# Performance work log

Measured on AMD Instinct MI355X. Metric: run time of the kernel, lower is better.

## Reference

```python
import jax, jax.numpy as jnp
import numpy as np

B, C, H, W = 8, 256, 64, 64
NH, FF, L, K = 8, 1024, 3, 64
THR = 0.5
DH = C // NH
SCALE = 1.0 / float(np.sqrt(DH))
N = H * W


def setup_inputs() -> dict:
    key = jax.random.key(0)
    ks = jax.random.split(key, 16)
    s = 0.02
    rn = lambda k, shape: (jax.random.normal(k, shape, jnp.float32) * s)
    return {
        "x": jax.random.normal(ks[0], (B, C, H, W), jnp.float32),
        "y": jax.random.normal(ks[1], (B, C, H, W), jnp.float32),
        "proj_w": rn(ks[2], (C, 2 * C)), "proj_b": rn(ks[3], (C,)),
        "sal_w": rn(ks[4], (1, C)), "sal_b": rn(ks[5], (1,)),
        "soft_w": rn(ks[6], (2, K, C)), "soft_b": rn(ks[7], (2, K)),
        "attn_in_w": rn(ks[8], (2, L, 3 * C, C)), "attn_in_b": rn(ks[9], (2, L, 3 * C)),
        "attn_out_w": rn(ks[10], (2, L, C, C)), "attn_out_b": rn(ks[11], (2, L, C)),
        "n1_g": jnp.ones((2, L, C), jnp.float32), "n1_b": jnp.zeros((2, L, C), jnp.float32),
        "ffn_w1": rn(ks[12], (2, L, FF, C)), "ffn_b1": rn(ks[13], (2, L, FF)),
        "ffn_w2": rn(ks[14], (2, L, C, FF)), "ffn_b2": rn(ks[15], (2, L, C)),
        "n2_g": jnp.ones((2, L, C), jnp.float32), "n2_b": jnp.zeros((2, L, C), jnp.float32),
    }


def _ln(t, g, b, eps=1e-5):
    m = t.mean(-1, keepdims=True)
    v = ((t - m) ** 2).mean(-1, keepdims=True)
    return (t - m) / jnp.sqrt(v + eps) * g + b


def _layers(q, kv, p, side):
    # q: [B,N,C] pixel queries, kv: [B,K,C] soft-pooled tokens
    for l in range(L):
        iw, ib = p["attn_in_w"][side, l], p["attn_in_b"][side, l]
        qq = (q @ iw[:C].T + ib[:C]).reshape(B, -1, NH, DH)
        kk = (kv @ iw[C:2 * C].T + ib[C:2 * C]).reshape(B, K, NH, DH)
        vv = (kv @ iw[2 * C:].T + ib[2 * C:]).reshape(B, K, NH, DH)
        att = jax.nn.softmax(jnp.einsum('bnhd,bkhd->bhnk', qq, kk) * SCALE, axis=-1)
        o = jnp.einsum('bhnk,bkhd->bnhd', att, vv).reshape(B, -1, C)
        o = o @ p["attn_out_w"][side, l].T + p["attn_out_b"][side, l]
        q = _ln(q + o, p["n1_g"][side, l], p["n1_b"][side, l])
        h = jax.nn.relu(q @ p["ffn_w1"][side, l].T + p["ffn_b1"][side, l])
        h = h @ p["ffn_w2"][side, l].T + p["ffn_b2"][side, l]
        q = _ln(q + h, p["n2_g"][side, l], p["n2_b"][side, l])
    return q


def _forward(x, y, proj_w, proj_b, sal_w, sal_b, soft_w, soft_b,
             attn_in_w, attn_in_b, attn_out_w, attn_out_b, n1_g, n1_b,
             ffn_w1, ffn_b1, ffn_w2, ffn_b2, n2_g, n2_b):
    p = dict(attn_in_w=attn_in_w, attn_in_b=attn_in_b, attn_out_w=attn_out_w,
             attn_out_b=attn_out_b, n1_g=n1_g, n1_b=n1_b, ffn_w1=ffn_w1,
             ffn_b1=ffn_b1, ffn_w2=ffn_w2, ffn_b2=ffn_b2, n2_g=n2_g, n2_b=n2_b)
    xc = jnp.concatenate([x, y], axis=1)                                  # [B,2C,H,W]
    feat = jnp.einsum('oc,bchw->bohw', proj_w, xc) + proj_b[None, :, None, None]
    sal = jnp.einsum('oc,bchw->bohw', sal_w, feat) + sal_b[None, :, None, None]  # [B,1,H,W]
    heat = jax.nn.sigmoid(sal)
    fg_mask = (heat >= THR).reshape(B, 1, N)
    bg_mask = (heat < 1.0 - THR).reshape(B, 1, N)
    fmap = feat.reshape(B, C, N)
    q0 = fmap.transpose(0, 2, 1)                                          # [B,N,C]
    out = fmap
    for side, hm in ((0, heat), (1, 1.0 - heat)):
        wf = feat * hm                                                    # [B,C,H,W]
        sw = (jnp.einsum('kc,bchw->bkhw', soft_w[side], wf)
              + soft_b[side][None, :, None, None]).reshape(B, K, N)       # [B,K,N]
        pool = jnp.einsum('bkn,bcn->bkc', sw, wf.reshape(B, C, N))        # [B,K,C]
        qs = _layers(q0, pool, p, side)                                   # [B,N,C]
        mask = fg_mask if side == 0 else bg_mask
        out = jnp.where(mask, qs.transpose(0, 2, 1), out)
    # per-image skip: if no fg or no bg pixels, keep original feature
    valid = fg_mask.any(axis=(1, 2)) & bg_mask.any(axis=(1, 2))           # [B]
    out = jnp.where(valid[:, None, None], out, fmap)
    return out.reshape(B, C, H, W)


def reference(x, y, proj_w, proj_b, sal_w, sal_b, soft_w, soft_b,
              attn_in_w, attn_in_b, attn_out_w, attn_out_b, n1_g, n1_b,
              ffn_w1, ffn_b1, ffn_w2, ffn_b2, n2_g, n2_b):
    return _forward(x, y, proj_w, proj_b, sal_w, sal_b, soft_w, soft_b,
                    attn_in_w, attn_in_b, attn_out_w, attn_out_b, n1_g, n1_b,
                    ffn_w1, ffn_b1, ffn_w2, ffn_b2, n2_g, n2_b)
```

## Files before the change

### kernel.cpp

```cpp
#include <hip/hip_runtime.h>
#include <stdint.h>

#define B_ 8
#define C_ 256
#define N_ 4096
#define K_ 64
#define NH_ 8
#define FF_ 1024
#define L_ 3
#define M_ (B_*N_)
#define SCALE_ 0.17677669529663687f

typedef float f32x4 __attribute__((ext_vector_type(4)));
typedef __bf16 v8bf __attribute__((ext_vector_type(8)));

__device__ __forceinline__ float b2f(unsigned short h){
  union { uint32_t u; float f; } v; v.u = ((uint32_t)h) << 16; return v.f;
}
__device__ __forceinline__ unsigned short f2b(float f){
  union { float f; uint32_t u; } v; v.f = f;
  uint32_t r = v.u + 0x7fffu + ((v.u >> 16) & 1u);
  return (unsigned short)(r >> 16);
}
__device__ __forceinline__ void gload_lds16(const void* g, void* l){
  __builtin_amdgcn_global_load_lds(
      (const __attribute__((address_space(1))) unsigned int*)g,
      (__attribute__((address_space(3))) unsigned int*)l, 16, 0, 0);
}
__device__ __forceinline__ void unpack8(uint4 v, float* o){
  o[0]=b2f((unsigned short)(v.x & 0xffff)); o[1]=b2f((unsigned short)(v.x >> 16));
  o[2]=b2f((unsigned short)(v.y & 0xffff)); o[3]=b2f((unsigned short)(v.y >> 16));
  o[4]=b2f((unsigned short)(v.z & 0xffff)); o[5]=b2f((unsigned short)(v.z >> 16));
  o[6]=b2f((unsigned short)(v.w & 0xffff)); o[7]=b2f((unsigned short)(v.w >> 16));
}

__global__ __launch_bounds__(256) void k_f32_to_bf16(const float* __restrict__ src,
                                                     unsigned short* __restrict__ dst, int n){
  int i4 = (blockIdx.x*256 + threadIdx.x)*4;
  if (i4 >= n) return;
  float4 v = *(const float4*)(src + i4);
  uint32_t p0 = (uint32_t)f2b(v.x) | ((uint32_t)f2b(v.y) << 16);
  uint32_t p1 = (uint32_t)f2b(v.z) | ((uint32_t)f2b(v.w) << 16);
  *(uint2*)(dst + i4) = make_uint2(p0, p1);
}

__global__ __launch_bounds__(256) void k_build_xcT(const float* __restrict__ x,
                                                   const float* __restrict__ y,
                                                   unsigned short* __restrict__ xcT){
  __shared__ float t[32][33];
  int b = blockIdx.z;
  int n0 = blockIdx.x*32, c0 = blockIdx.y*32;
  int tx = threadIdx.x, ty = threadIdx.y;
  const float* src = (c0 < 256) ? (x + ((size_t)b*256 + c0)*N_)
                                : (y + ((size_t)b*256 + (c0-256))*N_);
  #pragma unroll
  for (int i = 0; i < 4; i++){
    int cl = ty*4 + i;
    t[cl][tx] = src[(size_t)cl*N_ + n0 + tx];
  }
  __syncthreads();
  #pragma unroll
  for (int i = 0; i < 4; i++){
    int nl = ty*4 + i;
    xcT[((size_t)b*N_ + n0 + nl)*512 + c0 + tx] = f2b(t[tx][nl]);
  }
}

__global__ __launch_bounds__(256) void k_featmir(const float* __restrict__ featT,
                                                 unsigned short* __restrict__ featbf,
                                                 unsigned short* __restrict__ featC){
  __shared__ float t[32][33];
  int b = blockIdx.z;
  int n0 = blockIdx.x*32, c0 = blockIdx.y*32;
  int tx = threadIdx.x, ty = threadIdx.y;
  #pragma unroll
  for (int i = 0; i < 4; i++){
    int nl = ty*4 + i;
    size_t m = (size_t)b*N_ + n0 + nl;
    float v = featT[m*256 + c0 + tx];
    t[nl][tx] = v;
    featbf[m*256 + c0 + tx] = f2b(v);
  }
  __syncthreads();
  #pragma unroll
  for (int i = 0; i < 4; i++){
    int cl = ty*4 + i;
    featC[((size_t)b*256 + c0 + cl)*(size_t)N_ + n0 + tx] = f2b(t[tx][cl]);
  }
}

__global__ __launch_bounds__(512) void k_compute_u(const float* __restrict__ sal_w,
                                                   const float* __restrict__ proj_w,
                                                   const float* __restrict__ proj_b,
                                                   const float* __restrict__ sal_b,
                                                   double* __restrict__ u){
  int c2 = threadIdx.x;
  double acc = 0.0;
  for (int c = 0; c < 256; ++c)
    acc += (double)sal_w[c] * (double)proj_w[(size_t)c*512 + c2];
  u[c2] = acc;
  if (c2 == 0){
    double s0 = (double)sal_b[0];
    for (int c = 0; c < 256; ++c) s0 += (double)sal_w[c] * (double)proj_b[c];
    u[512] = s0;
  }
}

__global__ __launch_bounds__(256) void k_sal_part(const float* __restrict__ x,
                                                  const float* __restrict__ y,
                                                  const double* __restrict__ u,
                                                  double* __restrict__ part){
  int pix = blockIdx.x*256 + threadIdx.x;
  int cc = blockIdx.y;
  int b = pix >> 12, n = pix & 4095;
  int c0 = cc*32;
  const float* src = (c0 < 256) ? (x + ((size_t)b*256 + c0)*N_ + n)
                                : (y + ((size_t)b*256 + (c0-256))*N_ + n);
  const double* uu = u + c0;
  double acc = 0.0;
  #pragma unroll 8
  for (int c = 0; c < 32; ++c) acc += uu[c] * (double)src[(size_t)c*N_];
  part[(size_t)cc*32768 + pix] = acc;
}

__global__ __launch_bounds__(256) void k_sal_red(const double* __restrict__ part,
                                                 const double* __restrict__ u,
                                                 float* __restrict__ heat,
                                                 int* __restrict__ counts){
  int pix = blockIdx.x*256 + threadIdx.x;
  int b = pix >> 12;
  double acc = u[512];
  #pragma unroll
  for (int cc = 0; cc < 16; cc++) acc += part[(size_t)cc*32768 + pix];
  float hf = (float)(1.0 / (1.0 + exp(-acc)));
  heat[pix] = hf;
  unsigned long long mfg = __ballot(hf >= 0.5f);
  unsigned long long mbg = __ballot(hf < 0.5f);
  if ((threadIdx.x & 63) == 0){
    atomicAdd(&counts[b*2+0], (int)__popcll(mfg));
    atomicAdd(&counts[b*2+1], (int)__popcll(mbg));
  }
}

template<int EPI>
__global__ __launch_bounds__(256) void k_gemm_bt(
    const unsigned short* __restrict__ A, const unsigned short* __restrict__ W,
    const float* __restrict__ bias, void* __restrict__ out,
    int M, int N, int K){
  __shared__ unsigned short smem[2][2][128*64];
  int tid = threadIdx.x;
  int w = tid >> 6, l = tid & 63;
  int m0 = blockIdx.x * 128, n0 = blockIdx.y * 128;
  int wr = w >> 1, wc = w & 1;
  int lr = l & 15, lk = l >> 4;
  f32x4 acc[4][4] = {};
  int nt = K >> 6;
  #pragma unroll
  for (int i = 0; i < 4; i++){
    int idx = i*256 + tid;
    int row = idx >> 3, su = ((idx & 7) ^ (row & 7))*8;
    gload_lds16(A + (size_t)(m0+row)*K + su, &smem[0][0][idx*8]);
    gload_lds16(W + (size_t)(n0+row)*K + su, &smem[0][1][idx*8]);
  }
  __syncthreads();
  for (int t = 0; t < nt; ++t){
    int cur = t & 1;
    if (t + 1 < nt){
      int k0 = (t + 1) << 6;
      #pragma unroll
      for (int i = 0; i < 4; i++){
        int idx = i*256 + tid;
        int row = idx >> 3, su = ((idx & 7) ^ (row & 7))*8;
        gload_lds16(A + (size_t)(m0+row)*K + k0 + su, &smem[cur^1][0][idx*8]);
        gload_lds16(W + (size_t)(n0+row)*K + k0 + su, &smem[cur^1][1][idx*8]);
      }
    }
    const unsigned short* ldsA = smem[cur][0];
    const unsigned short* ldsB = smem[cur][1];
    #pragma unroll
    for (int kk = 0; kk < 2; kk++){
      v8bf af[4], bfr[4];
      #pragma unroll
      for (int f = 0; f < 4; f++){
        int ra = wr*64 + f*16 + lr;
        int rb2 = wc*64 + f*16 + lr;
        int u = kk*4 + lk;
        af[f]  = *(const v8bf*)(&ldsA[ra*64 + ((u ^ (ra&7))<<3)]);
        bfr[f] = *(const v8bf*)(&ldsB[rb2*64 + ((u ^ (rb2&7))<<3)]);
      }
      #pragma unroll
      for (int fi = 0; fi < 4; fi++)
        #pragma unroll
        for (int fj = 0; fj < 4; fj++)
          acc[fi][fj] = __builtin_amdgcn_mfma_f32_16x16x32_bf16(af[fi], bfr[fj], acc[fi][fj], 0, 0, 0);
    }
    __syncthreads();
  }
  if (EPI == 1 || EPI == 2){
    unsigned short* st = &smem[0][0][0];
    #pragma unroll
    for (int fj = 0; fj < 4; fj++){
      int col = wc*64 + fj*16 + lr;
      float bv = bias[n0 + col];
      #pragma unroll
      for (int fi = 0; fi < 4; fi++){
        int rl = wr*64 + fi*16 + lk*4;
        #pragma unroll
        for (int r = 0; r < 4; r++){
          float v = acc[fi][fj][r] + bv;
          if (EPI == 1) v = fmaxf(v, 0.f);
          st[(rl + r)*136 + col] = f2b(v);
        }
      }
    }
    __syncthreads();
    #pragma unroll
    for (int it = 0; it < 8; it++){
      int idx = it*256 + tid;
      int row = idx >> 4, c8 = (idx & 15)*8;
      *(uint4*)((unsigned short*)out + (size_t)(m0+row)*N + n0 + c8)
          = *(const uint4*)&st[row*136 + c8];
    }
  } else {
    #pragma unroll
    for (int fj = 0; fj < 4; fj++){
      int col = n0 + wc*64 + fj*16 + lr;
      float bv = bias[col];
      #pragma unroll
      for (int fi = 0; fi < 4; fi++){
        int rb = m0 + wr*64 + fi*16 + lk*4;
        #pragma unroll
        for (int r = 0; r < 4; r++){
          float v = acc[fi][fj][r] + bv;
          if (EPI == 3){
            int row = rb + r;
            ((unsigned short*)out)[((size_t)(row>>6)*256 + col)*64 + (row&63)] = f2b(v);
          } else {
            ((float*)out)[(size_t)(rb + r)*N + col] = v;
          }
        }
      }
    }
  }
}

__global__ __launch_bounds__(256) void k_kv(
    const unsigned short* __restrict__ pool, const unsigned short* __restrict__ iw,
    const float* __restrict__ ib, unsigned short* __restrict__ kk_bf,
    unsigned short* __restrict__ vvT_bf){
  __shared__ unsigned short smem[2][2][128*64];
  int tid = threadIdx.x;
  int w = tid >> 6, l = tid & 63;
  int m0 = blockIdx.x * 128, n0 = blockIdx.y * 128;
  int isv = blockIdx.z;
  const unsigned short* W = iw + (size_t)(isv ? 512 : 256)*256;
  const float* bias = ib + (isv ? 512 : 256);
  int wr = w >> 1, wc = w & 1;
  int lr = l & 15, lk = l >> 4;
  f32x4 acc[4][4] = {};
  #pragma unroll
  for (int i = 0; i < 4; i++){
    int idx = i*256 + tid;
    int row = idx >> 3, su = ((idx & 7) ^ (row & 7))*8;
    gload_lds16(pool + (size_t)(m0+row)*256 + su, &smem[0][0][idx*8]);
    gload_lds16(W + (size_t)(n0+row)*256 + su, &smem[0][1][idx*8]);
  }
  __syncthreads();
  for (int t = 0; t < 4; ++t){
    int cur = t & 1;
    if (t + 1 < 4){
      int k0 = (t + 1) << 6;
      #pragma unroll
      for (int i = 0; i < 4; i++){
        int idx = i*256 + tid;
        int row = idx >> 3, su = ((idx & 7) ^ (row & 7))*8;
        gload_lds16(pool + (size_t)(m0+row)*256 + k0 + su, &smem[cur^1][0][idx*8]);
        gload_lds16(W + (size_t)(n0+row)*256 + k0 + su, &smem[cur^1][1][idx*8]);
      }
    }
    const unsigned short* ldsA = smem[cur][0];
    const unsigned short* ldsB = smem[cur][1];
    #pragma unroll
    for (int kk = 0; kk < 2; kk++){
      v8bf af[4], bfr[4];
      #pragma unroll
      for (int f = 0; f < 4; f++){
        int ra = wr*64 + f*16 + lr;
        int rb2 = wc*64 + f*16 + lr;
        int u = kk*4 + lk;
        af[f]  = *(const v8bf*)(&ldsA[ra*64 + ((u ^ (ra&7))<<3)]);
        bfr[f] = *(const v8bf*)(&ldsB[rb2*64 + ((u ^ (rb2&7))<<3)]);
      }
      #pragma unroll
      for (int fi = 0; fi < 4; fi++)
        #pragma unroll
        for (int fj = 0; fj < 4; fj++)
          acc[fi][fj] = __builtin_amdgcn_mfma_f32_16x16x32_bf16(af[fi], bfr[fj], acc[fi][fj], 0, 0, 0);
    }
    __syncthreads();
  }
  #pragma unroll
  for (int fj = 0; fj < 4; fj++){
    int col = n0 + wc*64 + fj*16 + lr;
    float bv = bias[col];
    #pragma unroll
    for (int fi = 0; fi < 4; fi++){
      int rb = m0 + wr*64 + fi*16 + lk*4;
      #pragma unroll
      for (int r = 0; r < 4; r++){
        float v = acc[fi][fj][r] + bv;
        int row = rb + r;
        if (isv)
          vvT_bf[((size_t)(row>>6)*256 + col)*64 + (row&63)] = f2b(v);
        else
          kk_bf[(size_t)row*256 + col] = f2b(v);
      }
    }
  }
}

template<int RF32>
__global__ __launch_bounds__(512) void k_gemm_ln(
    const unsigned short* __restrict__ A, const unsigned short* __restrict__ W,
    const float* __restrict__ bias, const void* __restrict__ resid,
    const float* __restrict__ g, const float* __restrict__ bta,
    unsigned short* __restrict__ qout){
  __shared__ unsigned short smem[49152];
  int tid = threadIdx.x;
  int w = tid >> 6, l = tid & 63;
  int m0 = blockIdx.x * 128;
  int wm = w >> 2, wf = w & 3;
  int lr = l & 15, lk = l >> 4;
  f32x4 acc[4][4] = {};
  #pragma unroll
  for (int i = 0; i < 2; i++){
    int idx = i*512 + tid;
    int row = idx >> 3, su = ((idx & 7) ^ (row & 7))*8;
    gload_lds16(A + (size_t)(m0+row)*256 + su, &smem[idx*8]);
  }
  #pragma unroll
  for (int i = 0; i < 4; i++){
    int idx = i*512 + tid;
    int row = idx >> 3, su = ((idx & 7) ^ (row & 7))*8;
    gload_lds16(W + (size_t)row*256 + su, &smem[8192 + idx*8]);
  }
  __syncthreads();
  for (int t = 0; t < 4; ++t){
    int cur = t & 1;
    if (t + 1 < 4){
      int k0 = (t + 1) << 6;
      unsigned short* bA = smem + (cur^1)*24576;
      unsigned short* bB = bA + 8192;
      #pragma unroll
      for (int i = 0; i < 2; i++){
        int idx = i*512 + tid;
        int row = idx >> 3, su = ((idx & 7) ^ (row & 7))*8;
        gload_lds16(A + (size_t)(m0+row)*256 + k0 + su, &bA[idx*8]);
      }
      #pragma unroll
      for (int i = 0; i < 4; i++){
        int idx = i*512 + tid;
        int row = idx >> 3, su = ((idx & 7) ^ (row & 7))*8;
        gload_lds16(W + (size_t)row*256 + k0 + su, &bB[idx*8]);
      }
    }
    const unsigned short* bA = smem + cur*24576;
    const unsigned short* bB = bA + 8192;
    #pragma unroll
    for (int kk = 0; kk < 2; kk++){
      v8bf af[4], wb[4];
      int u = kk*4 + lk;
      #pragma unroll
      for (int f = 0; f < 4; f++){
        int ra = wm*64 + f*16 + lr;
        af[f] = *(const v8bf*)&bA[ra*64 + ((u ^ (ra&7))<<3)];
      }
      #pragma unroll
      for (int f = 0; f < 4; f++){
        int rc = wf*64 + f*16 + lr;
        wb[f] = *(const v8bf*)&bB[rc*64 + ((u ^ (rc&7))<<3)];
      }
      #pragma unroll
      for (int fi = 0; fi < 4; fi++)
        #pragma unroll
        for (int fc = 0; fc < 4; fc++)
          acc[fi][fc] = __builtin_amdgcn_mfma_f32_16x16x32_bf16(af[fi], wb[fc], acc[fi][fc], 0, 0, 0);
    }
    __syncthreads();
  }
  unsigned short* st = smem;
  #pragma unroll
  for (int fc = 0; fc < 4; fc++){
    int col = wf*64 + fc*16 + lr;
    float bv = bias[col];
    #pragma unroll
    for (int fi = 0; fi < 4; fi++){
      int rl = wm*64 + fi*16 + lk*4;
      #pragma unroll
      for (int r = 0; r < 4; r++)
        st[(rl + r)*264 + col] = f2b(acc[fi][fc][r] + bv);
    }
  }
  __syncthreads();
  int row = tid >> 2, seg = tid & 3;
  float xv[64];
  #pragma unroll
  for (int j = 0; j < 8; j++){
    int cu = seg*8 + j;
    uint4 dv = *(const uint4*)&st[row*264 + cu*8];
    float dd[8];
    unpack8(dv, dd);
    if (RF32){
      const float* rp = (const float*)resid + (size_t)(m0+row)*256 + cu*8;
      float4 r0 = *(const float4*)rp, r1 = *(const float4*)(rp + 4);
      xv[j*8+0] = r0.x + dd[0]; xv[j*8+1] = r0.y + dd[1];
      xv[j*8+2] = r0.z + dd[2]; xv[j*8+3] = r0.w + dd[3];
      xv[j*8+4] = r1.x + dd[4]; xv[j*8+5] = r1.y + dd[5];
      xv[j*8+6] = r1.z + dd[6]; xv[j*8+7] = r1.w + dd[7];
    } else {
      uint4 rv = *(const uint4*)((const unsigned short*)resid + (size_t)(m0+row)*256 + cu*8);
      float rr[8];
      unpack8(rv, rr);
      #pragma unroll
      for (int e = 0; e < 8; e++) xv[j*8+e] = rr[e] + dd[e];
    }
  }
  float s = 0.f, q = 0.f;
  #pragma unroll
  for (int i2 = 0; i2 < 64; i2++){ s += xv[i2]; q += xv[i2]*xv[i2]; }
  s += __shfl_xor(s, 1); s += __shfl_xor(s, 2);
  q += __shfl_xor(q, 1); q += __shfl_xor(q, 2);
  float mean = s * (1.0f/256.0f);
  float rstd = 1.0f / sqrtf(q*(1.0f/256.0f) - mean*mean + 1e-5f);
  #pragma unroll
  for (int j = 0; j < 8; j++){
    int c0 = seg*64 + j*8;
    float4 g0 = *(const float4*)(g + c0), g1 = *(const float4*)(g + c0 + 4);
    float4 b0 = *(const float4*)(bta + c0), b1 = *(const float4*)(bta + c0 + 4);
    float y0 = (xv[j*8+0]-mean)*rstd*g0.x + b0.x;
    float y1 = (xv[j*8+1]-mean)*rstd*g0.y + b0.y;
    float y2 = (xv[j*8+2]-mean)*rstd*g0.z + b0.z;
    float y3 = (xv[j*8+3]-mean)*rstd*g0.w + b0.w;
    float y4 = (xv[j*8+4]-mean)*rstd*g1.x + b1.x;
    float y5 = (xv[j*8+5]-mean)*rstd*g1.y + b1.y;
    float y6 = (xv[j*8+6]-mean)*rstd*g1.z + b1.z;
    float y7 = (xv[j*8+7]-mean)*rstd*g1.w + b1.w;
    uint4 ov;
    ov.x = (uint32_t)f2b(y0) | ((uint32_t)f2b(y1)<<16);
    ov.y = (uint32_t)f2b(y2) | ((uint32_t)f2b(y3)<<16);
    ov.z = (uint32_t)f2b(y4) | ((uint32_t)f2b(y5)<<16);
    ov.w = (uint32_t)f2b(y6) | ((uint32_t)f2b(y7)<<16);
    *(uint4*)(qout + (size_t)(m0+row)*256 + c0) = ov;
  }
}

__global__ __launch_bounds__(512) void k_ffn(
    const unsigned short* __restrict__ qb, const unsigned short* __restrict__ W1g,
    const float* __restrict__ b1g, const unsigned short* __restrict__ W2g,
    const float* __restrict__ b2g, const float* __restrict__ n2g,
    const float* __restrict__ n2b, unsigned short* __restrict__ qout){
  __shared__ unsigned short smem[73728];
  unsigned short* sA  = smem;
  unsigned short* sW1 = smem + 32768;
  unsigned short* sW2 = smem + 49152;
  unsigned short* sH  = smem + 65536;
  int tid = threadIdx.x;
  int w = tid >> 6, l = tid & 63;
  int m0 = blockIdx.x * 128;
  int wm = w >> 2, wf = w & 3;
  int lr = l & 15, lk = l >> 4;

  #pragma unroll
  for (int i = 0; i < 8; i++){
    int idx = i*512 + tid;
    int row = idx >> 5, gu = idx & 31;
    int su = (gu & 24) | ((gu & 7) ^ (row & 7));
    gload_lds16(qb + (size_t)(m0+row)*256 + su*8, &sA[idx*8]);
  }
  #pragma unroll
  for (int i = 0; i < 4; i++){
    int idx = i*512 + tid;
    int row = idx >> 5, gu = idx & 31;
    int su = (gu & 24) | ((gu & 7) ^ (row & 7));
    gload_lds16(W1g + (size_t)row*256 + su*8, &sW1[idx*8]);
  }
  #pragma unroll
  for (int i = 0; i < 4; i++){
    int idx = i*512 + tid;
    int row = idx >> 3, gu = idx & 7;
    int su = gu ^ (row & 7);
    gload_lds16(W2g + (size_t)row*1024 + su*8, &sW2[idx*8]);
  }
  __syncthreads();

  f32x4 acc[4][4] = {};
  for (int cc = 0; cc < 16; ++cc){
    f32x4 hacc[4] = {};
    #pragma unroll
    for (int ks = 0; ks < 8; ks++){
      int gu = ks*4 + lk;
      int rf = wf*16 + lr;
      v8bf bf1 = *(const v8bf*)&sW1[rf*256 + (((gu & 24) | ((gu & 7) ^ (rf & 7)))<<3)];
      #pragma unroll
      for (int f = 0; f < 4; f++){
        int ra = wm*64 + f*16 + lr;
        v8bf af = *(const v8bf*)&sA[ra*256 + (((gu & 24) | ((gu & 7) ^ (ra & 7)))<<3)];
        hacc[f] = __builtin_amdgcn_mfma_f32_16x16x32_bf16(af, bf1, hacc[f], 0, 0, 0);
      }
    }
    {
      int fc = wf*16 + lr;
      float b1v = b1g[cc*64 + fc];
      #pragma unroll
      for (int fi = 0; fi < 4; fi++){
        int mr0 = wm*64 + fi*16 + lk*4;
        #pragma unroll
        for (int r = 0; r < 4; r++){
          float v = fmaxf(hacc[fi][r] + b1v, 0.f);
          int mr = mr0 + r;
          int key = (mr ^ (mr >> 3)) & 7;
          sH[mr*64 + (((fc >> 3) ^ key)<<3) + (fc & 7)] = f2b(v);
        }
      }
    }
    __syncthreads();
    if (cc + 1 < 16){
      int f0n = (cc+1)*64;
      #pragma unroll
      for (int i = 0; i < 4; i++){
        int idx = i*512 + tid;
        int row = idx >> 5, gu = idx & 31;
        int su = (gu & 24) | ((gu & 7) ^ (row & 7));
        gload_lds16(W1g + (size_t)(f0n+row)*256 + su*8, &sW1[idx*8]);
      }
    }
    #pragma unroll
    for (int ks2 = 0; ks2 < 2; ks2++){
      int gu = ks2*4 + lk;
      v8bf ha[4], wb[4];
      #pragma unroll
      for (int f = 0; f < 4; f++){
        int rh = wm*64 + f*16 + lr;
        int key = (rh ^ (rh >> 3)) & 7;
        ha[f] = *(const v8bf*)&sH[rh*64 + ((gu ^ key)<<3)];
      }
      #pragma unroll
      for (int f = 0; f < 4; f++){
        int rc = wf*64 + f*16 + lr;
        wb[f] = *(const v8bf*)&sW2[rc*64 + ((gu ^ (rc & 7))<<3)];
      }
      #pragma unroll
      for (int fi = 0; fi < 4; fi++)
        #pragma unroll
        for (int fc = 0; fc < 4; fc++)
          acc[fi][fc] = __builtin_amdgcn_mfma_f32_16x16x32_bf16(ha[fi], wb[fc], acc[fi][fc], 0, 0, 0);
    }
    __syncthreads();
    if (cc + 1 < 16){
      int f0n = (cc+1)*64;
      #pragma unroll
      for (int i = 0; i < 4; i++){
        int idx = i*512 + tid;
        int row = idx >> 3, gu = idx & 7;
        int su = gu ^ (row & 7);
        gload_lds16(W2g + (size_t)row*1024 + f0n + su*8, &sW2[idx*8]);
      }
    }
  }

  unsigned short* st = smem + 32768;
  #pragma unroll
  for (int fc = 0; fc < 4; fc++){
    int col = wf*64 + fc*16 + lr;
    float bv = b2g[col];
    #pragma unroll
    for (int fi = 0; fi < 4; fi++){
      int rl = wm*64 + fi*16 + lk*4;
      #pragma unroll
      for (int r = 0; r < 4; r++)
        st[(rl + r)*264 + col] = f2b(acc[fi][fc][r] + bv);
    }
  }
  __syncthreads();
  int row = tid >> 2, seg = tid & 3;
  float xv[64];
  #pragma unroll
  for (int j = 0; j < 8; j++){
    int cu = seg*8 + j;
    int su = (cu & 24) | ((cu & 7) ^ (row & 7));
    uint4 rv = *(const uint4*)&sA[row*256 + su*8];
    uint4 dv = *(const uint4*)&st[row*264 + cu*8];
    float rr[8], dd[8];
    unpack8(rv, rr); unpack8(dv, dd);
    #pragma unroll
    for (int e = 0; e < 8; e++) xv[j*8+e] = rr[e] + dd[e];
  }
  float s = 0.f, q = 0.f;
  #pragma unroll
  for (int i2 = 0; i2 < 64; i2++){ s += xv[i2]; q += xv[i2]*xv[i2]; }
  s += __shfl_xor(s, 1); s += __shfl_xor(s, 2);
  q += __shfl_xor(q, 1); q += __shfl_xor(q, 2);
  float mean = s * (1.0f/256.0f);
  float rstd = 1.0f / sqrtf(q*(1.0f/256.0f) - mean*mean + 1e-5f);
  #pragma unroll
  for (int j = 0; j < 8; j++){
    int c0 = seg*64 + j*8;
    float4 g0 = *(const float4*)(n2g + c0), g1 = *(const float4*)(n2g + c0 + 4);
    float4 b0 = *(const float4*)(n2b + c0), b1 = *(const float4*)(n2b + c0 + 4);
    float y0 = (xv[j*8+0]-mean)*rstd*g0.x + b0.x;
    float y1 = (xv[j*8+1]-mean)*rstd*g0.y + b0.y;
    float y2 = (xv[j*8+2]-mean)*rstd*g0.z + b0.z;
    float y3 = (xv[j*8+3]-mean)*rstd*g0.w + b0.w;
    float y4 = (xv[j*8+4]-mean)*rstd*g1.x + b1.x;
    float y5 = (xv[j*8+5]-mean)*rstd*g1.y + b1.y;
    float y6 = (xv[j*8+6]-mean)*rstd*g1.z + b1.z;
    float y7 = (xv[j*8+7]-mean)*rstd*g1.w + b1.w;
    uint4 ov;
    ov.x = (uint32_t)f2b(y0) | ((uint32_t)f2b(y1)<<16);
    ov.y = (uint32_t)f2b(y2) | ((uint32_t)f2b(y3)<<16);
    ov.z = (uint32_t)f2b(y4) | ((uint32_t)f2b(y5)<<16);
    ov.w = (uint32_t)f2b(y6) | ((uint32_t)f2b(y7)<<16);
    *(uint4*)(qout + (size_t)(m0+row)*256 + c0) = ov;
  }
}

__global__ __launch_bounds__(256) void k_swh(const float* __restrict__ g_all,
                                             const float* __restrict__ heat,
                                             const float* __restrict__ soft_b,
                                             unsigned short* __restrict__ swh){
  __shared__ float gl[64*129];
  __shared__ float hml[64];
  int tid = threadIdx.x;
  int blk = blockIdx.x;
  size_t m0 = (size_t)blk*64;
  int b = (int)(m0 >> 12), n0 = (int)(m0 & 4095);
  #pragma unroll
  for (int i = 0; i < 32; i++){
    int idx = i*256 + tid;
    int row = idx >> 7, col = idx & 127;
    gl[row*129 + col] = g_all[(m0 + row)*128 + col];
  }
  if (tid < 64) hml[tid] = heat[(size_t)b*4096 + n0 + tid];
  __syncthreads();
  int k = tid >> 2, j0 = (tid & 3)*16;
  #pragma unroll
  for (int s = 0; s < 2; s++){
    float sb = soft_b[s*64 + k];
    unsigned short vals[16];
    #pragma unroll
    for (int j = 0; j < 16; j++){
      int n = j0 + j;
      float h = hml[n];
      float hm = s ? (1.0f - h) : h;
      vals[j] = f2b((gl[n*129 + s*64 + k]*hm + sb)*hm);
    }
    unsigned short* dst = swh + (((size_t)b*2 + s)*64 + k)*4096 + n0 + j0;
    uint4 o0, o1;
    o0.x = vals[0] | ((uint32_t)vals[1]<<16);  o0.y = vals[2] | ((uint32_t)vals[3]<<16);
    o0.z = vals[4] | ((uint32_t)vals[5]<<16);  o0.w = vals[6] | ((uint32_t)vals[7]<<16);
    o1.x = vals[8] | ((uint32_t)vals[9]<<16);  o1.y = vals[10]| ((uint32_t)vals[11]<<16);
    o1.z = vals[12]| ((uint32_t)vals[13]<<16); o1.w = vals[14]| ((uint32_t)vals[15]<<16);
    *(uint4*)dst = o0;
    *(uint4*)(dst + 8) = o1;
  }
}

__global__ __launch_bounds__(256) void k_poolgemm(
    const unsigned short* __restrict__ swh, const unsigned short* __restrict__ featC,
    float* __restrict__ pp){
  __shared__ unsigned short ldsA[128*64];
  __shared__ unsigned short ldsB[128*64];
  int tid = threadIdx.x;
  int w = tid >> 6, l = tid & 63;
  int kc = blockIdx.x, nt = blockIdx.y, b = blockIdx.z;
  int wr = w >> 1, wc = w & 1;
  int lr = l & 15, lk = l >> 4;
  const unsigned short* A = swh  + (size_t)b*128*4096 + kc*512;
  const unsigned short* W = featC + ((size_t)b*256 + nt*128)*4096 + kc*512;
  f32x4 acc[4][4] = {};
  for (int k0 = 0; k0 < 512; k0 += 64){
    #pragma unroll
    for (int i = 0; i < 4; i++){
      int idx = i*256 + tid;
      int row = idx >> 3, su = (idx & 7) ^ (row & 7);
      gload_lds16(A + (size_t)row*4096 + k0 + su*8, &ldsA[idx*8]);
    }
    #pragma unroll
    for (int i = 0; i < 4; i++){
      int idx = i*256 + tid;
      int row = idx >> 3, su = (idx & 7) ^ (row & 7);
      gload_lds16(W + (size_t)row*4096 + k0 + su*8, &ldsB[idx*8]);
    }
    __syncthreads();
    #pragma unroll
    for (int kk = 0; kk < 2; kk++){
      v8bf af[4], bfr[4];
      #pragma unroll
      for (int f = 0; f < 4; f++){
        int ra = wr*64 + f*16 + lr;
        int rb2 = wc*64 + f*16 + lr;
        int u = kk*4 + lk;
        af[f]  = *(const v8bf*)(&ldsA[ra*64 + ((u ^ (ra&7))<<3)]);
        bfr[f] = *(const v8bf*)(&ldsB[rb2*64 + ((u ^ (rb2&7))<<3)]);
      }
      #pragma unroll
      for (int fi = 0; fi < 4; fi++)
        #pragma unroll
        for (int fj = 0; fj < 4; fj++)
          acc[fi][fj] = __builtin_amdgcn_mfma_f32_16x16x32_bf16(af[fi], bfr[fj], acc[fi][fj], 0, 0, 0);
    }
    __syncthreads();
  }
  float* dst = pp + ((size_t)kc*8 + b)*128*256;
  #pragma unroll
  for (int fj = 0; fj < 4; fj++){
    int col = nt*128 + wc*64 + fj*16 + lr;
    #pragma unroll
    for (int fi = 0; fi < 4; fi++){
      int rb = wr*64 + fi*16 + lk*4;
      #pragma unroll
      for (int r = 0; r < 4; r++)
        dst[(size_t)(rb + r)*256 + col] = acc[fi][fj][r];
    }
  }
}

__global__ __launch_bounds__(256) void k_pool2b(const float* __restrict__ pp,
                                                unsigned short* __restrict__ pool_bf_s){
  int bk = blockIdx.x, side = blockIdx.y, c = threadIdx.x;
  int b = bk >> 6, k = bk & 63;
  float s = 0.f;
  #pragma unroll
  for (int kc = 0; kc < 8; kc++)
    s += pp[(((size_t)kc*8 + b)*128 + side*64 + k)*256 + c];
  pool_bf_s[((size_t)side*512 + bk)*256 + c] = f2b(s);
}

__global__ __launch_bounds__(256) void k_attn2(
    const unsigned short* __restrict__ qq, const unsigned short* __restrict__ kk,
    const unsigned short* __restrict__ vvT, unsigned short* __restrict__ obf){
  __shared__ unsigned short sk[64*256];
  __shared__ unsigned short svT[256*64];
  __shared__ unsigned short sp[4][16*64];
  __shared__ unsigned short sow[4][16*32];
  int tid = threadIdx.x, w = tid >> 6, l = tid & 63;
  int blk = blockIdx.x, b = blk >> 6;
  int l15 = l & 15, lg = l >> 4;
  const uint4* ksrc = (const uint4*)(kk + (size_t)b*64*256);
  #pragma unroll
  for (int i = 0; i < 8; i++){
    int u = i*256 + tid;
    int row = u >> 5, j = u & 31;
    *(uint4*)&sk[row*256 + ((j ^ (row&7))<<3)] = ksrc[u];
  }
  const uint4* vsrc = (const uint4*)(vvT + (size_t)b*256*64);
  #pragma unroll
  for (int i = 0; i < 8; i++){
    int u = i*256 + tid;
    int row = u >> 3, j = u & 7;
    *(uint4*)&svT[row*64 + ((j ^ (row&7))<<3)] = vsrc[u];
  }
  __syncthreads();
  size_t qrow = (size_t)blk*64 + w*16 + l15;
  for (int h = 0; h < 8; h++){
    v8bf aq = *(const v8bf*)(qq + qrow*256 + h*32 + lg*8);
    f32x4 s[4];
    #pragma unroll
    for (int kt = 0; kt < 4; kt++){
      int row = kt*16 + l15;
      v8bf bk = *(const v8bf*)&sk[row*256 + (((h*4 + lg) ^ (row&7))<<3)];
      f32x4 z = {};
      s[kt] = __builtin_amdgcn_mfma_f32_16x16x32_bf16(aq, bk, z, 0, 0, 0);
    }
    #pragma unroll
    for (int r = 0; r < 4; r++){
      float v0 = s[0][r]*SCALE_, v1 = s[1][r]*SCALE_;
      float v2 = s[2][r]*SCALE_, v3 = s[3][r]*SCALE_;
      float mx = fmaxf(fmaxf(v0, v1), fmaxf(v2, v3));
      mx = fmaxf(mx, __shfl_xor(mx, 1));
      mx = fmaxf(mx, __shfl_xor(mx, 2));
      mx = fmaxf(mx, __shfl_xor(mx, 4));
      mx = fmaxf(mx, __shfl_xor(mx, 8));
      float e0 = __expf(v0-mx), e1 = __expf(v1-mx);
      float e2 = __expf(v2-mx), e3 = __expf(v3-mx);
      float sum = e0+e1+e2+e3;
      sum += __shfl_xor(sum, 1); sum += __shfl_xor(sum, 2);
      sum += __shfl_xor(sum, 4); sum += __shfl_xor(sum, 8);
      float inv = 1.0f/sum;
      s[0][r] = e0*inv; s[1][r] = e1*inv; s[2][r] = e2*inv; s[3][r] = e3*inv;
    }
    #pragma unroll
    for (int kt = 0; kt < 4; kt++){
      int colu = kt*2 + (l15>>3);
      #pragma unroll
      for (int r = 0; r < 4; r++){
        int row = lg*4 + r;
        sp[w][row*64 + ((colu ^ (row&7))<<3) + (l&7)] = f2b(s[kt][r]);
      }
    }
    f32x4 o[2] = {};
    #pragma unroll
    for (int k2 = 0; k2 < 2; k2++){
      v8bf pa = *(const v8bf*)&sp[w][l15*64 + (((k2*4 + lg) ^ (l15&7))<<3)];
      #pragma unroll
      for (int dt = 0; dt < 2; dt++){
        int vrow = h*32 + dt*16 + l15;
        v8bf bv = *(const v8bf*)&svT[vrow*64 + (((k2*4 + lg) ^ (vrow&7))<<3)];
        o[dt] = __builtin_amdgcn_mfma_f32_16x16x32_bf16(pa, bv, o[dt], 0, 0, 0);
      }
    }
    #pragma unroll
    for (int dt = 0; dt < 2; dt++)
      #pragma unroll
      for (int r = 0; r < 4; r++)
        sow[w][(lg*4 + r)*32 + dt*16 + l15] = f2b(o[dt][r]);
    uint4 ov = *(const uint4*)&sow[w][l15*32 + lg*8];
    *(uint4*)(obf + qrow*256 + h*32 + lg*8) = ov;
  }
}

__global__ __launch_bounds__(256) void k_select(
    const unsigned short* __restrict__ qA, const unsigned short* __restrict__ qB,
    const float* __restrict__ featT, const float* __restrict__ heat,
    const int* __restrict__ counts, float* __restrict__ out){
  __shared__ float t[32][33];
  int b = blockIdx.z;
  int n0 = blockIdx.x*32, c0 = blockIdx.y*32;
  int tx = threadIdx.x, ty = threadIdx.y;
  bool valid = (counts[b*2] > 0) && (counts[b*2+1] > 0);
  #pragma unroll
  for (int i = 0; i < 4; i++){
    int nl = ty*4+i;
    size_t m = (size_t)b*4096 + n0 + nl;
    float v;
    if (!valid) v = featT[m*256 + c0 + tx];
    else {
      bool fg = heat[(size_t)b*4096 + n0 + nl] >= 0.5f;
      v = fg ? b2f(qA[m*256 + c0 + tx]) : b2f(qB[m*256 + c0 + tx]);
    }
    t[nl][tx] = v;
  }
  __syncthreads();
  #pragma unroll
  for (int i = 0; i < 4; i++){
    int cl = ty*4+i;
    out[((size_t)b*256 + c0 + cl)*4096 + n0 + tx] = t[tx][cl];
  }
}

extern "C" void kernel_launch(void* const* d_in, const int* in_sizes, int n_in,
                              void* d_out, int out_size, void* d_ws, size_t ws_size,
                              hipStream_t stream){
  const float* x         = (const float*)d_in[0];
  const float* y         = (const float*)d_in[1];
  const float* proj_w    = (const float*)d_in[2];
  const float* proj_b    = (const float*)d_in[3];
  const float* sal_w     = (const float*)d_in[4];
  const float* sal_b     = (const float*)d_in[5];
  const float* soft_w    = (const float*)d_in[6];
  const float* soft_b    = (const float*)d_in[7];
  const float* attn_in_w = (const float*)d_in[8];
  const float* attn_in_b = (const float*)d_in[9];
  const float* attn_out_w= (const float*)d_in[10];
  const float* attn_out_b= (const float*)d_in[11];
  const float* n1_g      = (const float*)d_in[12];
  const float* n1_b      = (const float*)d_in[13];
  const float* ffn_w1    = (const float*)d_in[14];
  const float* ffn_b1    = (const float*)d_in[15];
  const float* ffn_w2    = (const float*)d_in[16];
  const float* ffn_b2    = (const float*)d_in[17];
  const float* n2_g      = (const float*)d_in[18];
  const float* n2_b      = (const float*)d_in[19];
  float* out = (float*)d_out;

  char* p = (char*)d_ws;
  auto alloc = [&](size_t bytes){ char* r = p; p += (bytes + 255) & ~(size_t)255; return r; };
  unsigned short* hbf   = (unsigned short*)alloc((size_t)M_*FF_*2);
  unsigned short* xcT   = hbf;
  unsigned short* qq_bf = hbf;
  float* featT = (float*)alloc((size_t)M_*C_*4);
  unsigned short* qAb = (unsigned short*)alloc((size_t)M_*C_*2);
  unsigned short* swh = qAb;
  unsigned short* qBb = (unsigned short*)alloc((size_t)M_*C_*2);
  unsigned short* obf = (unsigned short*)alloc((size_t)M_*C_*2);
  unsigned short* featC = obf;
  unsigned short* featbf = (unsigned short*)alloc((size_t)M_*C_*2);
  unsigned short* tmpb = (unsigned short*)alloc((size_t)M_*C_*2);
  float* g_all = (float*)tmpb;
  float* pp    = (float*)alloc((size_t)8*8*128*256*4);
  double* salp = (double*)pp;
  unsigned short* pool_bf_s = (unsigned short*)alloc((size_t)2*512*256*2);
  unsigned short* kk_bf = (unsigned short*)alloc((size_t)B_*K_*C_*2);
  unsigned short* vvT_bf= (unsigned short*)alloc((size_t)B_*C_*K_*2);
  float* heat = (float*)alloc((size_t)B_*N_*4);
  double* u   = (double*)alloc(513*8);
  int* counts = (int*)alloc(64);
  float* zbias = (float*)alloc(512);
  unsigned short* projw_bf = (unsigned short*)alloc((size_t)C_*512*2);
  unsigned short* aiw_bf = (unsigned short*)alloc((size_t)2*L_*768*C_*2);
  unsigned short* aow_bf = (unsigned short*)alloc((size_t)2*L_*C_*C_*2);
  unsigned short* f1w_bf = (unsigned short*)alloc((size_t)2*L_*FF_*C_*2);
  unsigned short* f2w_bf = (unsigned short*)alloc((size_t)2*L_*C_*FF_*2);
  unsigned short* sw2_bf = (unsigned short*)alloc((size_t)2*K_*C_*2);

  hipMemsetAsync(counts, 0, 64, stream);
  hipMemsetAsync(zbias, 0, 512, stream);
  k_compute_u<<<1, 512, 0, stream>>>(sal_w, proj_w, proj_b, sal_b, u);
  k_sal_part<<<dim3(128, 16), 256, 0, stream>>>(x, y, u, salp);
  k_sal_red<<<128, 256, 0, stream>>>(salp, u, heat, counts);

  auto conv = [&](const float* s, unsigned short* d, size_t n){
    k_f32_to_bf16<<<(unsigned)((n/4 + 255)/256), 256, 0, stream>>>(s, d, (int)n);
  };
  conv(proj_w,     projw_bf, (size_t)C_*512);
  conv(attn_in_w,  aiw_bf,   (size_t)2*L_*768*C_);
  conv(attn_out_w, aow_bf,   (size_t)2*L_*C_*C_);
  conv(ffn_w1,     f1w_bf,   (size_t)2*L_*FF_*C_);
  conv(ffn_w2,     f2w_bf,   (size_t)2*L_*C_*FF_);
  conv(soft_w,     sw2_bf,   (size_t)2*K_*C_);

  k_build_xcT<<<dim3(N_/32, 512/32, B_), dim3(32,8), 0, stream>>>(x, y, xcT);
  k_gemm_bt<0><<<dim3(M_/128, C_/128), 256, 0, stream>>>(xcT, projw_bf, proj_b, featT, M_, C_, 512);
  k_featmir<<<dim3(N_/32, C_/32, B_), dim3(32,8), 0, stream>>>(featT, featbf, featC);

  k_gemm_bt<0><<<dim3(M_/128, 1), 256, 0, stream>>>(featbf, sw2_bf, zbias, g_all, M_, 128, C_);
  k_swh<<<M_/64, 256, 0, stream>>>(g_all, heat, soft_b, swh);
  k_poolgemm<<<dim3(8, 2, B_), 256, 0, stream>>>(swh, featC, pp);
  k_pool2b<<<dim3(512, 2), 256, 0, stream>>>(pp, pool_bf_s);

  for (int side = 0; side < 2; ++side){
    unsigned short* qb = side ? qBb : qAb;
    const unsigned short* poolS = pool_bf_s + (size_t)side*512*256;
    for (int lyr = 0; lyr < L_; ++lyr){
      int sl = side*L_ + lyr;
      const unsigned short* iw = aiw_bf + (size_t)sl*768*C_;
      const float* ib = attn_in_b + (size_t)sl*768;
      const unsigned short* qin = (lyr == 0) ? featbf : qb;
      k_gemm_bt<2><<<dim3(M_/128, C_/128), 256, 0, stream>>>(qin, iw, ib, qq_bf, M_, C_, C_);
      k_kv<<<dim3(4, 2, 2), 256, 0, stream>>>(poolS, iw, ib, kk_bf, vvT_bf);
      k_attn2<<<M_/64, 256, 0, stream>>>(qq_bf, kk_bf, vvT_bf, obf);
      if (lyr == 0)
        k_gemm_ln<1><<<M_/128, 512, 0, stream>>>(obf, aow_bf + (size_t)sl*C_*C_,
            attn_out_b + (size_t)sl*C_, featT, n1_g + (size_t)sl*C_, n1_b + (size_t)sl*C_, qb);
      else
        k_gemm_ln<0><<<M_/128, 512, 0, stream>>>(obf, aow_bf + (size_t)sl*C_*C_,
            attn_out_b + (size_t)sl*C_, qb, n1_g + (size_t)sl*C_, n1_b + (size_t)sl*C_, qb);
      k_ffn<<<M_/128, 512, 0, stream>>>(qb, f1w_bf + (size_t)sl*FF_*C_, ffn_b1 + (size_t)sl*FF_,
                                        f2w_bf + (size_t)sl*C_*FF_, ffn_b2 + (size_t)sl*C_,
                                        n2_g + (size_t)sl*C_, n2_b + (size_t)sl*C_, qb);
    }
  }
  k_select<<<dim3(N_/32, C_/32, B_), dim3(32,8), 0, stream>>>(qAb, qBb, featT, heat, counts, out);
}
```

Measured before the change: 917.9 us.

## Split FFN residual+LayerNorm into separate kernel and stage outputs through LDS

Removes the fused residual-add and LayerNorm epilogue from the FFN kernel. The FFN kernel now writes its bias-added output to a temporary buffer, and a new per-row wave kernel (k_ln2) does the residual add and LayerNorm. The gemm_ln epilogue and the FFN store now stage results in LDS and write them out as coalesced rows, and the sH swizzle key is simplified. The goal is lower register pressure and better stores in the FFN kernel. The cost is an extra launch plus a full round trip of the activation tensor through global memory for each layer.

```diff
diff --git a/kernel.cpp b/kernel.cpp
--- a/kernel.cpp
+++ b/kernel.cpp
@@ -437,28 +437,30 @@
     int c0 = seg*64 + j*8;
     float4 g0 = *(const float4*)(g + c0), g1 = *(const float4*)(g + c0 + 4);
     float4 b0 = *(const float4*)(bta + c0), b1 = *(const float4*)(bta + c0 + 4);
-    float y0 = (xv[j*8+0]-mean)*rstd*g0.x + b0.x;
-    float y1 = (xv[j*8+1]-mean)*rstd*g0.y + b0.y;
-    float y2 = (xv[j*8+2]-mean)*rstd*g0.z + b0.z;
-    float y3 = (xv[j*8+3]-mean)*rstd*g0.w + b0.w;
-    float y4 = (xv[j*8+4]-mean)*rstd*g1.x + b1.x;
-    float y5 = (xv[j*8+5]-mean)*rstd*g1.y + b1.y;
-    float y6 = (xv[j*8+6]-mean)*rstd*g1.z + b1.z;
-    float y7 = (xv[j*8+7]-mean)*rstd*g1.w + b1.w;
     uint4 ov;
-    ov.x = (uint32_t)f2b(y0) | ((uint32_t)f2b(y1)<<16);
-    ov.y = (uint32_t)f2b(y2) | ((uint32_t)f2b(y3)<<16);
-    ov.z = (uint32_t)f2b(y4) | ((uint32_t)f2b(y5)<<16);
-    ov.w = (uint32_t)f2b(y6) | ((uint32_t)f2b(y7)<<16);
-    *(uint4*)(qout + (size_t)(m0+row)*256 + c0) = ov;
+    ov.x = (uint32_t)f2b((xv[j*8+0]-mean)*rstd*g0.x + b0.x)
+         | ((uint32_t)f2b((xv[j*8+1]-mean)*rstd*g0.y + b0.y) << 16);
+    ov.y = (uint32_t)f2b((xv[j*8+2]-mean)*rstd*g0.z + b0.z)
+         | ((uint32_t)f2b((xv[j*8+3]-mean)*rstd*g0.w + b0.w) << 16);
+    ov.z = (uint32_t)f2b((xv[j*8+4]-mean)*rstd*g1.x + b1.x)
+         | ((uint32_t)f2b((xv[j*8+5]-mean)*rstd*g1.y + b1.y) << 16);
+    ov.w = (uint32_t)f2b((xv[j*8+6]-mean)*rstd*g1.z + b1.z)
+         | ((uint32_t)f2b((xv[j*8+7]-mean)*rstd*g1.w + b1.w) << 16);
+    *(uint4*)&st[row*264 + c0] = ov;
+  }
+  __syncthreads();
+  #pragma unroll
+  for (int it = 0; it < 8; it++){
+    int idx = it*512 + tid;
+    int rw = idx >> 5, c8 = (idx & 31)*8;
+    *(uint4*)(qout + (size_t)(m0+rw)*256 + c8) = *(const uint4*)&st[rw*264 + c8];
   }
 }
 
 __global__ __launch_bounds__(512) void k_ffn(
     const unsigned short* __restrict__ qb, const unsigned short* __restrict__ W1g,
     const float* __restrict__ b1g, const unsigned short* __restrict__ W2g,
-    const float* __restrict__ b2g, const float* __restrict__ n2g,
-    const float* __restrict__ n2b, unsigned short* __restrict__ qout){
+    const float* __restrict__ b2g, unsigned short* __restrict__ outb){
   __shared__ unsigned short smem[73728];
   unsigned short* sA  = smem;
   unsigned short* sW1 = smem + 32768;
@@ -467,28 +469,29 @@
   int tid = threadIdx.x;
   int w = tid >> 6, l = tid & 63;
   int m0 = blockIdx.x * 128;
-  int wm = w >> 2, wf = w & 3;
+  int wm = w >> 2;
+  int wf = w & 3;
   int lr = l & 15, lk = l >> 4;
 
   #pragma unroll
   for (int i = 0; i < 8; i++){
     int idx = i*512 + tid;
-    int row = idx >> 5, gu = idx & 31;
-    int su = (gu & 24) | ((gu & 7) ^ (row & 7));
+    int row = idx >> 5, g = idx & 31;
+    int su = (g & 24) | ((g & 7) ^ (row & 7));
     gload_lds16(qb + (size_t)(m0+row)*256 + su*8, &sA[idx*8]);
   }
   #pragma unroll
   for (int i = 0; i < 4; i++){
     int idx = i*512 + tid;
-    int row = idx >> 5, gu = idx & 31;
-    int su = (gu & 24) | ((gu & 7) ^ (row & 7));
+    int row = idx >> 5, g = idx & 31;
+    int su = (g & 24) | ((g & 7) ^ (row & 7));
     gload_lds16(W1g + (size_t)row*256 + su*8, &sW1[idx*8]);
   }
   #pragma unroll
   for (int i = 0; i < 4; i++){
     int idx = i*512 + tid;
-    int row = idx >> 3, gu = idx & 7;
-    int su = gu ^ (row & 7);
+    int row = idx >> 3, g = idx & 7;
+    int su = g ^ (row & 7);
     gload_lds16(W2g + (size_t)row*1024 + su*8, &sW2[idx*8]);
   }
   __syncthreads();
@@ -498,13 +501,13 @@
     f32x4 hacc[4] = {};
     #pragma unroll
     for (int ks = 0; ks < 8; ks++){
-      int gu = ks*4 + lk;
+      int g = ks*4 + lk;
       int rf = wf*16 + lr;
-      v8bf bf1 = *(const v8bf*)&sW1[rf*256 + (((gu & 24) | ((gu & 7) ^ (rf & 7)))<<3)];
+      v8bf bf1 = *(const v8bf*)&sW1[rf*256 + (((g & 24) | ((g & 7) ^ (rf & 7)))<<3)];
       #pragma unroll
       for (int f = 0; f < 4; f++){
         int ra = wm*64 + f*16 + lr;
-        v8bf af = *(const v8bf*)&sA[ra*256 + (((gu & 24) | ((gu & 7) ^ (ra & 7)))<<3)];
+        v8bf af = *(const v8bf*)&sA[ra*256 + (((g & 24) | ((g & 7) ^ (ra & 7)))<<3)];
         hacc[f] = __builtin_amdgcn_mfma_f32_16x16x32_bf16(af, bf1, hacc[f], 0, 0, 0);
       }
     }
@@ -518,8 +521,7 @@
         for (int r = 0; r < 4; r++){
           float v = fmaxf(hacc[fi][r] + b1v, 0.f);
           int mr = mr0 + r;
-          int key = (mr ^ (mr >> 3)) & 7;
-          sH[mr*64 + (((fc >> 3) ^ key)<<3) + (fc & 7)] = f2b(v);
+          sH[mr*64 + (((fc >> 3) ^ (mr & 7))<<3) + (fc & 7)] = f2b(v);
         }
       }
     }
@@ -529,25 +531,24 @@
       #pragma unroll
       for (int i = 0; i < 4; i++){
         int idx = i*512 + tid;
-        int row = idx >> 5, gu = idx & 31;
-        int su = (gu & 24) | ((gu & 7) ^ (row & 7));
+        int row = idx >> 5, g = idx & 31;
+        int su = (g & 24) | ((g & 7) ^ (row & 7));
         gload_lds16(W1g + (size_t)(f0n+row)*256 + su*8, &sW1[idx*8]);
       }
     }
     #pragma unroll
     for (int ks2 = 0; ks2 < 2; ks2++){
-      int gu = ks2*4 + lk;
+      int g = ks2*4 + lk;
       v8bf ha[4], wb[4];
       #pragma unroll
       for (int f = 0; f < 4; f++){
         int rh = wm*64 + f*16 + lr;
-        int key = (rh ^ (rh >> 3)) & 7;
-        ha[f] = *(const v8bf*)&sH[rh*64 + ((gu ^ key)<<3)];
+        ha[f] = *(const v8bf*)&sH[rh*64 + ((g ^ (rh & 7))<<3)];
       }
       #pragma unroll
       for (int f = 0; f < 4; f++){
         int rc = wf*64 + f*16 + lr;
-        wb[f] = *(const v8bf*)&sW2[rc*64 + ((gu ^ (rc & 7))<<3)];
+        wb[f] = *(const v8bf*)&sW2[rc*64 + ((g ^ (rc & 7))<<3)];
       }
       #pragma unroll
       for (int fi = 0; fi < 4; fi++)
@@ -561,14 +562,13 @@
       #pragma unroll
       for (int i = 0; i < 4; i++){
         int idx = i*512 + tid;
-        int row = idx >> 3, gu = idx & 7;
-        int su = gu ^ (row & 7);
+        int row = idx >> 3, g = idx & 7;
+        int su = g ^ (row & 7);
         gload_lds16(W2g + (size_t)row*1024 + f0n + su*8, &sW2[idx*8]);
       }
     }
   }
-
-  unsigned short* st = smem + 32768;
+  unsigned short* st = smem;
   #pragma unroll
   for (int fc = 0; fc < 4; fc++){
     int col = wf*64 + fc*16 + lr;
@@ -582,45 +582,11 @@
     }
   }
   __syncthreads();
-  int row = tid >> 2, seg = tid & 3;
-  float xv[64];
-  #pragma unroll
-  for (int j = 0; j < 8; j++){
-    int cu = seg*8 + j;
-    int su = (cu & 24) | ((cu & 7) ^ (row & 7));
-    uint4 rv = *(const uint4*)&sA[row*256 + su*8];
-    uint4 dv = *(const uint4*)&st[row*264 + cu*8];
-    float rr[8], dd[8];
-    unpack8(rv, rr); unpack8(dv, dd);
-    #pragma unroll
-    for (int e = 0; e < 8; e++) xv[j*8+e] = rr[e] + dd[e];
-  }
-  float s = 0.f, q = 0.f;
-  #pragma unroll
-  for (int i2 = 0; i2 < 64; i2++){ s += xv[i2]; q += xv[i2]*xv[i2]; }
-  s += __shfl_xor(s, 1); s += __shfl_xor(s, 2);
-  q += __shfl_xor(q, 1); q += __shfl_xor(q, 2);
-  float mean = s * (1.0f/256.0f);
-  float rstd = 1.0f / sqrtf(q*(1.0f/256.0f) - mean*mean + 1e-5f);
-  #pragma unroll
-  for (int j = 0; j < 8; j++){
-    int c0 = seg*64 + j*8;
-    float4 g0 = *(const float4*)(n2g + c0), g1 = *(const float4*)(n2g + c0 + 4);
-    float4 b0 = *(const float4*)(n2b + c0), b1 = *(const float4*)(n2b + c0 + 4);
-    float y0 = (xv[j*8+0]-mean)*rstd*g0.x + b0.x;
-    float y1 = (xv[j*8+1]-mean)*rstd*g0.y + b0.y;
-    float y2 = (xv[j*8+2]-mean)*rstd*g0.z + b0.z;
-    float y3 = (xv[j*8+3]-mean)*rstd*g0.w + b0.w;
-    float y4 = (xv[j*8+4]-mean)*rstd*g1.x + b1.x;
-    float y5 = (xv[j*8+5]-mean)*rstd*g1.y + b1.y;
-    float y6 = (xv[j*8+6]-mean)*rstd*g1.z + b1.z;
-    float y7 = (xv[j*8+7]-mean)*rstd*g1.w + b1.w;
-    uint4 ov;
-    ov.x = (uint32_t)f2b(y0) | ((uint32_t)f2b(y1)<<16);
-    ov.y = (uint32_t)f2b(y2) | ((uint32_t)f2b(y3)<<16);
-    ov.z = (uint32_t)f2b(y4) | ((uint32_t)f2b(y5)<<16);
-    ov.w = (uint32_t)f2b(y6) | ((uint32_t)f2b(y7)<<16);
-    *(uint4*)(qout + (size_t)(m0+row)*256 + c0) = ov;
+  #pragma unroll
+  for (int it = 0; it < 8; it++){
+    int idx = it*512 + tid;
+    int row = idx >> 5, c8 = (idx & 31)*8;
+    *(uint4*)(outb + (size_t)(m0+row)*256 + c8) = *(const uint4*)&st[row*264 + c8];
   }
 }
 
@@ -817,6 +783,48 @@
     uint4 ov = *(const uint4*)&sow[w][l15*32 + lg*8];
     *(uint4*)(obf + qrow*256 + h*32 + lg*8) = ov;
   }
+}
+
+template<int RF32>
+__global__ __launch_bounds__(256) void k_ln2(
+    const void* __restrict__ resid, const unsigned short* __restrict__ delta,
+    const float* __restrict__ g, const float* __restrict__ bta,
+    unsigned short* __restrict__ qout){
+  int wv = threadIdx.x >> 6, l = threadIdx.x & 63;
+  size_t m = (size_t)blockIdx.x*4 + wv;
+  uint2 dv = *(const uint2*)(delta + m*256 + l*4);
+  float d0 = b2f((unsigned short)(dv.x & 0xffff)), d1 = b2f((unsigned short)(dv.x >> 16));
+  float d2 = b2f((unsigned short)(dv.y & 0xffff)), d3 = b2f((unsigned short)(dv.y >> 16));
+  float x0, x1, x2, x3;
+  if (RF32){
+    float4 rv = *(const float4*)((const float*)resid + m*256 + l*4);
+    x0 = rv.x+d0; x1 = rv.y+d1; x2 = rv.z+d2; x3 = rv.w+d3;
+  } else {
+    uint2 rv = *(const uint2*)((const unsigned short*)resid + m*256 + l*4);
+    x0 = b2f((unsigned short)(rv.x & 0xffff)) + d0;
+    x1 = b2f((unsigned short)(rv.x >> 16)) + d1;
+    x2 = b2f((unsigned short)(rv.y & 0xffff)) + d2;
+    x3 = b2f((unsigned short)(rv.y >> 16)) + d3;
+  }
+  float s = x0+x1+x2+x3;
+  float ss = x0*x0+x1*x1+x2*x2+x3*x3;
+  #pragma unroll
+  for (int off = 32; off; off >>= 1){
+    s  += __shfl_xor(s, off);
+    ss += __shfl_xor(ss, off);
+  }
+  float mean = s * (1.0f/256.0f);
+  float var = ss * (1.0f/256.0f) - mean*mean;
+  float rstd = 1.0f / sqrtf(var + 1e-5f);
+  float4 gv = *(const float4*)(g + l*4);
+  float4 bv = *(const float4*)(bta + l*4);
+  float y0 = (x0-mean)*rstd*gv.x + bv.x;
+  float y1 = (x1-mean)*rstd*gv.y + bv.y;
+  float y2 = (x2-mean)*rstd*gv.z + bv.z;
+  float y3 = (x3-mean)*rstd*gv.w + bv.w;
+  uint32_t p0 = (uint32_t)f2b(y0) | ((uint32_t)f2b(y1)<<16);
+  uint32_t p1 = (uint32_t)f2b(y2) | ((uint32_t)f2b(y3)<<16);
+  *(uint2*)(qout + m*256 + l*4) = make_uint2(p0,p1);
 }
 
 __global__ __launch_bounds__(256) void k_select(
@@ -946,8 +954,8 @@
         k_gemm_ln<0><<<M_/128, 512, 0, stream>>>(obf, aow_bf + (size_t)sl*C_*C_,
             attn_out_b + (size_t)sl*C_, qb, n1_g + (size_t)sl*C_, n1_b + (size_t)sl*C_, qb);
       k_ffn<<<M_/128, 512, 0, stream>>>(qb, f1w_bf + (size_t)sl*FF_*C_, ffn_b1 + (size_t)sl*FF_,
-                                        f2w_bf + (size_t)sl*C_*FF_, ffn_b2 + (size_t)sl*C_,
-                                        n2_g + (size_t)sl*C_, n2_b + (size_t)sl*C_, qb);
+                                        f2w_bf + (size_t)sl*C_*FF_, ffn_b2 + (size_t)sl*C_, tmpb);
+      k_ln2<0><<<M_/4, 256, 0, stream>>>(qb, tmpb, n2_g + (size_t)sl*C_, n2_b + (size_t)sl*C_, qb);
     }
   }
   k_select<<<dim3(N_/32, C_/32, B_), dim3(32,8), 0, stream>>>(qAb, qBb, featT, heat, counts, out);
```

After: 875.4 us. 4.6% less time.
